# Performance work log

Measured on AMD Instinct MI355X. Metric: run time of the kernel, lower is better.

## Reference

```python
import jax, jax.numpy as jnp
import numpy as np

L = 65536
D = 256

def setup_inputs() -> dict:
    key = jax.random.key(0)
    k1, k2, k3 = jax.random.split(key, 3)
    K = jax.random.normal(k1, (L, D), dtype=jnp.float32)
    V = jax.random.normal(k2, (L, D), dtype=jnp.float32)
    q = jax.random.normal(k3, (D,), dtype=jnp.float32)  # nn.Parameter(torch.randn(d_model))
    return {"K": K, "V": V, "q": q, "mode": 0}

def reference(K, V, q, mode):
    # s[i] = <K[i], q>; online-softmax recurrence over the sequence dim.
    s = K @ q  # [L]
    neg_inf = jnp.float32(-jnp.inf)

    def step(carry, inp):
        m_prev, u_prev, w_prev = carry
        s_i, v_i = inp
        m = jnp.maximum(m_prev, s_i)
        e_prev = jnp.exp(m_prev - m)
        e_curr = jnp.exp(s_i - m)
        u = u_prev * e_prev + e_curr
        w = w_prev * e_prev + v_i * e_curr  # [D]
        return (m, u, w), w / u

    init = (neg_inf, jnp.float32(0.0), jnp.zeros((D,), dtype=V.dtype))
    _, out = jax.lax.scan(step, init, (s, V))  # out: [L, D]
    return out
```

## Files before the change

kernel.cpp:

```cpp
#include <hip/hip_runtime.h>
#include <math.h>

#define L_TOTAL 65536
#define D_DIM   256
#define C_ROWS  32
#define N_CHUNK (L_TOTAL / C_ROWS)
#define SUPER   32
#define N_SUPER (N_CHUNK / SUPER)

typedef float vf4 __attribute__((ext_vector_type(4)));

__global__ __launch_bounds__(256) void kA_aggregate(
    const float* __restrict__ K, const float* __restrict__ V,
    const float* __restrict__ q,
    float* __restrict__ s_g, float* __restrict__ cm,
    float* __restrict__ cu, float* __restrict__ cw)
{
    const int t = threadIdx.x;
    const int c = blockIdx.x;
    const int r0 = c * C_ROWS;
    const int wave = t >> 6, lane = t & 63;

    __shared__ float s_lds[C_ROWS];

    float v[C_ROWS];
    const float* Vp = V + (size_t)r0 * D_DIM + t;
    #pragma unroll
    for (int j = 0; j < C_ROWS; ++j) v[j] = Vp[(size_t)j * D_DIM];

    const vf4 q4 = *reinterpret_cast<const vf4*>(q + 4 * lane);
    const float* Kp = K + (size_t)(r0 + wave * 8) * D_DIM + 4 * lane;
    vf4 kv[8];
    #pragma unroll
    for (int k = 0; k < 8; ++k)
        kv[k] = __builtin_nontemporal_load(
                    reinterpret_cast<const vf4*>(Kp + (size_t)k * D_DIM));

    #pragma unroll
    for (int k = 0; k < 8; ++k) {
        float d = kv[k].x * q4.x + kv[k].y * q4.y + kv[k].z * q4.z + kv[k].w * q4.w;
        #pragma unroll
        for (int off = 32; off > 0; off >>= 1) d += __shfl_xor(d, off, 64);
        if (lane == 0) s_lds[wave * 8 + k] = d;
    }
    __syncthreads();

    if (t < C_ROWS) s_g[r0 + t] = s_lds[t];

    float m_c = -INFINITY;
    #pragma unroll
    for (int j = 0; j < C_ROWS; ++j) m_c = fmaxf(m_c, s_lds[j]);

    float u_c = 0.f, w = 0.f;
    #pragma unroll
    for (int j = 0; j < C_ROWS; ++j) {
        const float cf = __expf(s_lds[j] - m_c);
        u_c += cf;
        w = fmaf(cf, v[j], w);
    }

    cw[(size_t)c * D_DIM + t] = w;
    if (t == 0) { cm[c] = m_c; cu[c] = u_c; }
}

__global__ __launch_bounds__(256) void kCB_scan(
    const float* __restrict__ cm, const float* __restrict__ cu,
    const float* __restrict__ cw,
    float* __restrict__ pm, float* __restrict__ pu,
    float* __restrict__ gsup,
    float* __restrict__ pwl, float* __restrict__ T)
{
    const int t = threadIdx.x;
    const int S = blockIdx.x;
    __shared__ float Lm[256], Lu[256];
    __shared__ float pmL[N_CHUNK + 1];
    __shared__ float ca[SUPER], cb[SUPER];

    float am[8], au[8];
    float M = -INFINITY, U = 0.f;
    #pragma unroll
    for (int j = 0; j < 8; ++j) {
        am[j] = cm[8 * t + j]; au[j] = cu[8 * t + j];
        const float mm = fmaxf(M, am[j]);
        U = U * __expf(M - mm) + au[j] * __expf(am[j] - mm);
        M = mm;
    }
    Lm[t] = M; Lu[t] = U;
    float Mi = M, Ui = U;
    __syncthreads();
    for (int off = 1; off < 256; off <<= 1) {
        float m1 = 0.f, u1 = 0.f;
        const bool act = (t >= off);
        if (act) { m1 = Lm[t - off]; u1 = Lu[t - off]; }
        __syncthreads();
        if (act) {
            const float mm = fmaxf(m1, Mi);
            Ui = u1 * __expf(m1 - mm) + Ui * __expf(Mi - mm);
            Mi = mm;
            Lm[t] = Mi; Lu[t] = Ui;
        }
        __syncthreads();
    }
    float Me = (t == 0) ? -INFINITY : Lm[t - 1];
    float Ue = (t == 0) ? 0.f : Lu[t - 1];
    #pragma unroll
    for (int j = 0; j < 8; ++j) {
        pmL[8 * t + j] = Me;
        if (S == 0) { pm[8 * t + j] = Me; pu[8 * t + j] = Ue; }
        const float mm = fmaxf(Me, am[j]);
        Ue = Ue * __expf(Me - mm) + au[j] * __expf(am[j] - mm);
        Me = mm;
    }
    if (t == 255) {
        pmL[N_CHUNK] = Me;
        if (S == 0) { pm[N_CHUNK] = Me; pu[N_CHUNK] = Ue; }
    }
    __syncthreads();

    float wv[SUPER];
    const float* cwp = cw + (size_t)S * SUPER * D_DIM + t;
    #pragma unroll
    for (int j = 0; j < SUPER; ++j) wv[j] = cwp[(size_t)j * D_DIM];

    if (t < SUPER) {
        const int c = S * SUPER + t;
        ca[t] = __expf(pmL[c] - pmL[c + 1]);
        cb[t] = __expf(cm[c] - pmL[c + 1]);
    }
    if (t == 0)
        gsup[S] = __expf(pmL[S * SUPER] - pmL[S * SUPER + SUPER]);
    __syncthreads();

    float PW = 0.f;
    float* pwlp = pwl + (size_t)S * SUPER * D_DIM + t;
    #pragma unroll
    for (int j = 0; j < SUPER; ++j) {
        pwlp[(size_t)j * D_DIM] = PW;
        PW = PW * ca[j] + wv[j] * cb[j];
    }
    T[(size_t)S * D_DIM + t] = PW;
}

__global__ __launch_bounds__(256) void kF_output(
    const float* __restrict__ V, const float* __restrict__ s_g,
    const float* __restrict__ pm, const float* __restrict__ pu,
    const float* __restrict__ pwl, const float* __restrict__ T,
    const float* __restrict__ gsup,
    float* __restrict__ out)
{
    const int t = threadIdx.x;
    const int c = blockIdx.x;
    const int S = c / SUPER;
    const int r0 = c * C_ROWS;
    const int wave = t >> 6, lane = t & 63;

    __shared__ float sa[C_ROWS], se[C_ROWS], sri[C_ROWS];
    __shared__ float gl[N_SUPER];

    float v[C_ROWS];
    const float* Vp = V + (size_t)r0 * D_DIM + t;
    #pragma unroll
    for (int j = 0; j < C_ROWS; ++j) v[j] = Vp[(size_t)j * D_DIM];

    const float seed_pwl = pwl[(size_t)c * D_DIM + t];
    const float pmc = pm[c];
    const float pmS = pm[S * SUPER];

    if (t < N_SUPER) gl[t] = gsup[t];

    if (wave == 0) {
        const float puc = pu[c];
        float s_val = -INFINITY;
        if (lane < C_ROWS) s_val = s_g[r0 + lane];
        float m = s_val, u = 1.0f;
        #pragma unroll
        for (int off = 1; off < C_ROWS; off <<= 1) {
            const float m1 = __shfl_up(m, off, 32);
            const float u1 = __shfl_up(u, off, 32);
            if ((lane & 31) >= off) {
                const float mm = fmaxf(m1, m);
                u = u1 * __expf(m1 - mm) + u * __expf(m - mm);
                m = mm;
            }
        }
        const float m_row = fmaxf(pmc, m);
        const float u_row = puc * __expf(pmc - m_row) + u * __expf(m - m_row);
        const float m_prev_raw = __shfl_up(m_row, 1, 32);
        const float m_prev = ((lane & 31) == 0) ? pmc : m_prev_raw;
        if (lane < C_ROWS) {
            sa[lane]  = __expf(m_prev - m_row);
            se[lane]  = __expf(s_val - m_row);
            sri[lane] = 1.0f / u_row;
        }
    }
    __syncthreads();

    float SW = 0.f;
    const float* Tp = T + t;
    #pragma unroll 8
    for (int Sp = 0; Sp < S; ++Sp)
        SW = SW * gl[Sp] + Tp[(size_t)Sp * D_DIM];

    const float gf = (c == 0) ? 0.f : __expf(pmS - pmc);
    float W = SW * gf + seed_pwl;

    float* Op = out + (size_t)r0 * D_DIM + t;
    #pragma unroll
    for (int j = 0; j < C_ROWS; ++j) {
        W = W * sa[j] + v[j] * se[j];
        __builtin_nontemporal_store(W * sri[j], Op + (size_t)j * D_DIM);
    }
}

extern "C" void kernel_launch(void* const* d_in, const int* in_sizes, int n_in,
                              void* d_out, int out_size, void* d_ws, size_t ws_size,
                              hipStream_t stream) {
    const float* K = (const float*)d_in[0];
    const float* V = (const float*)d_in[1];
    const float* q = (const float*)d_in[2];
    float* out = (float*)d_out;

    float* ws   = (float*)d_ws;
    float* s_g  = ws;
    float* cm   = s_g + L_TOTAL;
    float* cu   = cm + N_CHUNK;
    float* pm   = cu + N_CHUNK;
    float* pu   = pm + (N_CHUNK + 16);
    float* gsup = pu + (N_CHUNK + 16);
    float* cw   = gsup + 128;
    float* pwl  = cw + (size_t)N_CHUNK * D_DIM;
    float* T    = pwl + (size_t)N_CHUNK * D_DIM;

    kA_aggregate<<<N_CHUNK, 256, 0, stream>>>(K, V, q, s_g, cm, cu, cw);
    kCB_scan<<<N_SUPER, 256, 0, stream>>>(cm, cu, cw, pm, pu, gsup, pwl, T);
    kF_output<<<N_CHUNK, 256, 0, stream>>>(V, s_g, pm, pu, pwl, T, gsup, out);
}
```

Before: 181.6 us.

## Vectorize V loads as float4 per wave-row and split chunk scan across waves

```diff
diff --git a/kernel.cpp b/kernel.cpp
--- a/kernel.cpp
+++ b/kernel.cpp
@@ -22,23 +22,19 @@
     const int wave = t >> 6, lane = t & 63;
 
     __shared__ float s_lds[C_ROWS];
-
-    float v[C_ROWS];
-    const float* Vp = V + (size_t)r0 * D_DIM + t;
-    #pragma unroll
-    for (int j = 0; j < C_ROWS; ++j) v[j] = Vp[(size_t)j * D_DIM];
+    __shared__ vf4  pw_lds[4][64];
+
+    vf4 v4[8];
+    const vf4* Vp = reinterpret_cast<const vf4*>(V + (size_t)(r0 + wave * 8) * D_DIM) + lane;
+    #pragma unroll
+    for (int k = 0; k < 8; ++k) v4[k] = Vp[(size_t)k * (D_DIM / 4)];
 
     const vf4 q4 = *reinterpret_cast<const vf4*>(q + 4 * lane);
-    const float* Kp = K + (size_t)(r0 + wave * 8) * D_DIM + 4 * lane;
-    vf4 kv[8];
-    #pragma unroll
-    for (int k = 0; k < 8; ++k)
-        kv[k] = __builtin_nontemporal_load(
-                    reinterpret_cast<const vf4*>(Kp + (size_t)k * D_DIM));
-
-    #pragma unroll
-    for (int k = 0; k < 8; ++k) {
-        float d = kv[k].x * q4.x + kv[k].y * q4.y + kv[k].z * q4.z + kv[k].w * q4.w;
+    const vf4* Kp = reinterpret_cast<const vf4*>(K + (size_t)(r0 + wave * 8) * D_DIM) + lane;
+    #pragma unroll
+    for (int k = 0; k < 8; ++k) {
+        const vf4 kv = __builtin_nontemporal_load(Kp + (size_t)k * (D_DIM / 4));
+        float d = kv.x * q4.x + kv.y * q4.y + kv.z * q4.z + kv.w * q4.w;
         #pragma unroll
         for (int off = 32; off > 0; off >>= 1) d += __shfl_xor(d, off, 64);
         if (lane == 0) s_lds[wave * 8 + k] = d;
@@ -50,16 +46,23 @@
     float m_c = -INFINITY;
     #pragma unroll
     for (int j = 0; j < C_ROWS; ++j) m_c = fmaxf(m_c, s_lds[j]);
-
-    float u_c = 0.f, w = 0.f;
-    #pragma unroll
-    for (int j = 0; j < C_ROWS; ++j) {
-        const float cf = __expf(s_lds[j] - m_c);
-        u_c += cf;
-        w = fmaf(cf, v[j], w);
-    }
-
-    cw[(size_t)c * D_DIM + t] = w;
+    float u_c = 0.f;
+    #pragma unroll
+    for (int j = 0; j < C_ROWS; ++j) u_c += __expf(s_lds[j] - m_c);
+
+    vf4 pw = {0.f, 0.f, 0.f, 0.f};
+    #pragma unroll
+    for (int k = 0; k < 8; ++k) {
+        const float cf = __expf(s_lds[wave * 8 + k] - m_c);
+        pw = pw + cf * v4[k];
+    }
+    pw_lds[wave][lane] = pw;
+    __syncthreads();
+
+    if (t < 64) {
+        const vf4 w4 = (pw_lds[0][t] + pw_lds[1][t]) + (pw_lds[2][t] + pw_lds[3][t]);
+        reinterpret_cast<vf4*>(cw + (size_t)c * D_DIM)[t] = w4;
+    }
     if (t == 0) { cm[c] = m_c; cu[c] = u_c; }
 }
 
@@ -155,20 +158,17 @@
     const int wave = t >> 6, lane = t & 63;
 
     __shared__ float sa[C_ROWS], se[C_ROWS], sri[C_ROWS];
-    __shared__ float gl[N_SUPER];
-
-    float v[C_ROWS];
-    const float* Vp = V + (size_t)r0 * D_DIM + t;
-    #pragma unroll
-    for (int j = 0; j < C_ROWS; ++j) v[j] = Vp[(size_t)j * D_DIM];
-
-    const float seed_pwl = pwl[(size_t)c * D_DIM + t];
-    const float pmc = pm[c];
-    const float pmS = pm[S * SUPER];
-
-    if (t < N_SUPER) gl[t] = gsup[t];
+    __shared__ vf4 seedL[64];
+    __shared__ vf4 seg[4][64];
+    __shared__ float asL[4];
+
+    vf4 v4[8];
+    const vf4* Vp = reinterpret_cast<const vf4*>(V + (size_t)(r0 + wave * 8) * D_DIM) + lane;
+    #pragma unroll
+    for (int k = 0; k < 8; ++k) v4[k] = Vp[(size_t)k * (D_DIM / 4)];
 
     if (wave == 0) {
+        const float pmc = pm[c];
         const float puc = pu[c];
         float s_val = -INFINITY;
         if (lane < C_ROWS) s_val = s_g[r0 + lane];
@@ -192,23 +192,45 @@
             se[lane]  = __expf(s_val - m_row);
             sri[lane] = 1.0f / u_row;
         }
-    }
-    __syncthreads();
-
-    float SW = 0.f;
-    const float* Tp = T + t;
-    #pragma unroll 8
-    for (int Sp = 0; Sp < S; ++Sp)
-        SW = SW * gl[Sp] + Tp[(size_t)Sp * D_DIM];
-
-    const float gf = (c == 0) ? 0.f : __expf(pmS - pmc);
-    float W = SW * gf + seed_pwl;
-
-    float* Op = out + (size_t)r0 * D_DIM + t;
-    #pragma unroll
-    for (int j = 0; j < C_ROWS; ++j) {
-        W = W * sa[j] + v[j] * se[j];
-        __builtin_nontemporal_store(W * sri[j], Op + (size_t)j * D_DIM);
+    } else if (wave == 1) {
+        const float pmc = pm[c];
+        const float pmS = pm[S * SUPER];
+        vf4 SW = {0.f, 0.f, 0.f, 0.f};
+        const vf4* T4 = reinterpret_cast<const vf4*>(T) + lane;
+        #pragma unroll 8
+        for (int Sp = 0; Sp < S; ++Sp) {
+            const float g = gsup[Sp];
+            SW = SW * g + T4[(size_t)Sp * (D_DIM / 4)];
+        }
+        const float gf = (c == 0) ? 0.f : __expf(pmS - pmc);
+        const vf4 sp = reinterpret_cast<const vf4*>(pwl + (size_t)c * D_DIM)[lane];
+        seedL[lane] = SW * gf + sp;
+    }
+    __syncthreads();
+
+    vf4 B = {0.f, 0.f, 0.f, 0.f};
+    float A = 1.f;
+    #pragma unroll
+    for (int k = 0; k < 8; ++k) {
+        const int j = wave * 8 + k;
+        B = B * sa[j] + v4[k] * se[j];
+        A *= sa[j];
+    }
+    seg[wave][lane] = B;
+    if (lane == 0) asL[wave] = A;
+    __syncthreads();
+
+    vf4 W = seedL[lane];
+    for (int p = 0; p < wave; ++p)
+        W = W * asL[p] + seg[p][lane];
+
+    float* Op = out + (size_t)(r0 + wave * 8) * D_DIM + 4 * lane;
+    #pragma unroll
+    for (int k = 0; k < 8; ++k) {
+        const int j = wave * 8 + k;
+        W = W * sa[j] + v4[k] * se[j];
+        __builtin_nontemporal_store(W * sri[j],
+                                    reinterpret_cast<vf4*>(Op + (size_t)k * D_DIM));
     }
 }
 
```

Measured after the change: 185.3 us. About the same (+2.0%).
